# Kernel tuning notes

Measured on AMD Instinct MI355X. Metric: run time of the kernel, lower is better.

The kernel has to match this reference:

```python
import jax, jax.numpy as jnp
import numpy as np

B, T, F, H, OUT, L = 4096, 336, 12, 50, 1, 3


def _lstm_layer(x_tbf, W_ih, W_hh, b_ih, b_hh):
    """PyTorch-semantics LSTM layer. x_tbf: [T,B,in]; returns [T,B,H]."""
    Hh = W_hh.shape[1]
    Bsz = x_tbf.shape[1]
    # precompute input projection for all timesteps: [T,B,4H]
    xz = jnp.einsum('tbf,gf->tbg', x_tbf, W_ih) + (b_ih + b_hh)

    def step(carry, xz_t):
        h, c = carry
        z = xz_t + h @ W_hh.T  # [B,4H]
        i, f, g, o = jnp.split(z, 4, axis=-1)  # PyTorch gate order i,f,g,o
        c = jax.nn.sigmoid(f) * c + jax.nn.sigmoid(i) * jnp.tanh(g)
        h = jax.nn.sigmoid(o) * jnp.tanh(c)
        return (h, c), h

    h0 = jnp.zeros((Bsz, Hh), x_tbf.dtype)
    c0 = jnp.zeros((Bsz, Hh), x_tbf.dtype)
    _, hs = jax.lax.scan(step, (h0, c0), xz)
    return hs


def setup_inputs() -> dict:
    key = jax.random.key(0)
    ks = jax.random.split(key, 16)
    s = 1.0 / np.sqrt(H)  # PyTorch LSTM init scale
    inp = {"x": jax.random.normal(ks[0], (B, T, F), dtype=jnp.float32)}
    in_sizes = [F, H, H]
    k = 1
    for l in range(L):
        inp[f"W_ih_{l}"] = jax.random.uniform(ks[k], (4 * H, in_sizes[l]), jnp.float32, -s, s); k += 1
        inp[f"W_hh_{l}"] = jax.random.uniform(ks[k], (4 * H, H), jnp.float32, -s, s); k += 1
        inp[f"b_ih_{l}"] = jax.random.uniform(ks[k], (4 * H,), jnp.float32, -s, s); k += 1
        inp[f"b_hh_{l}"] = jax.random.uniform(ks[k], (4 * H,), jnp.float32, -s, s); k += 1
    inp["W_lin"] = jax.random.uniform(ks[13], (OUT, H), jnp.float32, -s, s)
    inp["b_lin"] = jax.random.uniform(ks[14], (OUT,), jnp.float32, -s, s)
    return inp


def reference(x, W_ih_0, W_hh_0, b_ih_0, b_hh_0,
              W_ih_1, W_hh_1, b_ih_1, b_hh_1,
              W_ih_2, W_hh_2, b_ih_2, b_hh_2,
              W_lin, b_lin):
    h = jnp.transpose(x, (1, 0, 2))  # [T,B,F] time-major for scan
    params = [(W_ih_0, W_hh_0, b_ih_0, b_hh_0),
              (W_ih_1, W_hh_1, b_ih_1, b_hh_1),
              (W_ih_2, W_hh_2, b_ih_2, b_hh_2)]
    for W_ih, W_hh, bi, bh in params:
        h = _lstm_layer(h, W_ih, W_hh, bi, bh)  # [T,B,H]
    last = h[-1]  # out[:, -1, :] in batch_first layout
    return last @ W_lin.T + b_lin  # [B,OUT]
```

## Files before the change

### kernel.cpp

```cpp
#include <hip/hip_runtime.h>


#define Bsz 4096
#define Tt  336
#define BT  16
#define NTH 1024

typedef _Float16 half8 __attribute__((ext_vector_type(8)));
typedef float    floatx4 __attribute__((ext_vector_type(4)));

struct __align__(16) SMem {
  _Float16 act0[2][BT * 64];
  _Float16 act1[2][BT * 64];
  _Float16 act2[2][BT * 64];
};

__device__ __forceinline__ int offA(int n, int L) {
  return n * 64 + ((((L >> 3) ^ n) & 7) << 3) + (L & 7);
}

__device__ __forceinline__ float lstm_cell(floatx4 z, float& c) {
  float ei = __builtin_amdgcn_exp2f(z[0]);
  float ef = __builtin_amdgcn_exp2f(z[1]);
  float eg = __builtin_amdgcn_exp2f(z[2]);
  float eo = __builtin_amdgcn_exp2f(z[3]);
  float ig = __builtin_amdgcn_rcpf(1.f + ei);
  float fg = __builtin_amdgcn_rcpf(1.f + ef);
  float rg = __builtin_amdgcn_rcpf(1.f + eg);
  float og = __builtin_amdgcn_rcpf(1.f + eo);
  float gg = 1.f - 2.f * rg;
  c = fg * c + ig * gg;
  float ec = __builtin_amdgcn_exp2f(2.885390082f * c);
  float rc = __builtin_amdgcn_rcpf(1.f + ec);
  return og * (1.f - 2.f * rc);
}

__device__ __forceinline__ half8 wfrag2(const float* __restrict__ Wa, int lena,
                                        const float* __restrict__ Wb, int offb,
                                        int lenb, int R, int k0) {
  half8 r = {};
  int u = R >> 2, g = R & 3;
  float sc = (g == 2) ? 2.885390082f : -1.442695041f;
  if (u < 50) {
    int row = g * 50 + u;
#pragma unroll
    for (int j = 0; j < 8; ++j) {
      int k = k0 + j;
      float v = 0.f;
      if (Wa && k < lena)                         v = Wa[row * lena + k];
      else if (Wb && k >= offb && k < offb + lenb) v = Wb[row * lenb + (k - offb)];
      r[j] = (_Float16)(sc * v);
    }
  }
  return r;
}

#define MFMA(a, b, acc) __builtin_amdgcn_mfma_f32_16x16x32_f16((a), (b), (acc), 0, 0, 0)

#define CELLS(NCC, b0, b1, sw)                                          \
  {                                                                     \
    floatx4 z0 = bia[0], z1 = bia[1], z2 = bia[2];                      \
    z0 = MFMA(af[0][0], b0, z0);                                        \
    z1 = MFMA(af[1][0], b0, z1);                                        \
    if (NCC == 3) z2 = MFMA(af[2][0], b0, z2);                          \
    z0 = MFMA(af[0][1], b1, z0);                                        \
    z1 = MFMA(af[1][1], b1, z1);                                        \
    if (NCC == 3) z2 = MFMA(af[2][1], b1, z2);                          \
    float h0v = lstm_cell(z0, cst[0]);                                  \
    float h1v = lstm_cell(z1, cst[1]);                                  \
    if (uokk[0]) (sw)[wo[0]] = (_Float16)h0v;                           \
    if (uokk[1]) (sw)[wo[1]] = (_Float16)h1v;                           \
    if (NCC == 3) {                                                     \
      float h2v = lstm_cell(z2, cst[2]);                                \
      if (uokk[2]) (sw)[wo[2]] = (_Float16)h2v;                         \
    }                                                                   \
  }

#define CELLSD(NCC, b0, b1, pp, sw)                                     \
  {                                                                     \
    floatx4 z0 = bia[0], z1 = bia[1], z2 = bia[2];                      \
    z0 = MFMA(af[0][2], bpf[pp][0], z0);                                \
    z1 = MFMA(af[1][2], bpf[pp][0], z1);                                \
    if (NCC == 3) z2 = MFMA(af[2][2], bpf[pp][0], z2);                  \
    z0 = MFMA(af[0][3], bpf[pp][1], z0);                                \
    z1 = MFMA(af[1][3], bpf[pp][1], z1);                                \
    if (NCC == 3) z2 = MFMA(af[2][3], bpf[pp][1], z2);                  \
    z0 = MFMA(af[0][0], b0, z0);                                        \
    z1 = MFMA(af[1][0], b0, z1);                                        \
    if (NCC == 3) z2 = MFMA(af[2][0], b0, z2);                          \
    z0 = MFMA(af[0][1], b1, z0);                                        \
    z1 = MFMA(af[1][1], b1, z1);                                        \
    if (NCC == 3) z2 = MFMA(af[2][1], b1, z2);                          \
    float h0v = lstm_cell(z0, cst[0]);                                  \
    float h1v = lstm_cell(z1, cst[1]);                                  \
    if (uokk[0]) (sw)[wo[0]] = (_Float16)h0v;                           \
    if (uokk[1]) (sw)[wo[1]] = (_Float16)h1v;                           \
    if (NCC == 3) {                                                     \
      float h2v = lstm_cell(z2, cst[2]);                                \
      if (uokk[2]) (sw)[wo[2]] = (_Float16)h2v;                         \
    }                                                                   \
  }

__global__ __launch_bounds__(NTH, 4)
void lstm_mfma_kernel(const float* __restrict__ x,
                      const float* __restrict__ Wih0, const float* __restrict__ Whh0,
                      const float* __restrict__ bih0, const float* __restrict__ bhh0,
                      const float* __restrict__ Wih1, const float* __restrict__ Whh1,
                      const float* __restrict__ bih1, const float* __restrict__ bhh1,
                      const float* __restrict__ Wih2, const float* __restrict__ Whh2,
                      const float* __restrict__ bih2, const float* __restrict__ bhh2,
                      const float* __restrict__ Wlin, const float* __restrict__ blin,
                      float* __restrict__ out) {
  __shared__ SMem sm;
  const int tid  = threadIdx.x;
  const int blk  = blockIdx.x;
  const int lane = tid & 63;
  const int w    = tid >> 6;
  const int n    = lane & 15;
  const int q    = lane >> 4;

  {
    int* zp = (int*)&sm;
    for (int i = tid; i < (int)(sizeof(SMem) / 4); i += NTH) zp[i] = 0;
  }

  int Lw, nc, mm3[3] = {0, 0, 0};
  switch (w) {
    case 0:  Lw = 0; nc = 3; mm3[0] = 0;  mm3[1] = 1;  mm3[2] = 2;  break;
    case 1:  Lw = 0; nc = 2; mm3[0] = 3;  mm3[1] = 4;               break;
    case 2:  Lw = 0; nc = 3; mm3[0] = 5;  mm3[1] = 6;  mm3[2] = 7;  break;
    case 3:  Lw = 0; nc = 2; mm3[0] = 8;  mm3[1] = 9;               break;
    case 4:  Lw = 1; nc = 2; mm3[0] = 0;  mm3[1] = 1;               break;
    case 5:  Lw = 1; nc = 3; mm3[0] = 2;  mm3[1] = 3;  mm3[2] = 4;  break;
    case 6:  Lw = 1; nc = 2; mm3[0] = 5;  mm3[1] = 6;               break;
    case 7:  Lw = 1; nc = 3; mm3[0] = 7;  mm3[1] = 8;  mm3[2] = 9;  break;
    case 8:  Lw = 2; nc = 3; mm3[0] = 0;  mm3[1] = 1;  mm3[2] = 2;  break;
    case 9:  Lw = 2; nc = 2; mm3[0] = 3;  mm3[1] = 4;               break;
    case 10: Lw = 2; nc = 2; mm3[0] = 5;  mm3[1] = 6;               break;
    case 11: Lw = 2; nc = 2; mm3[0] = 7;  mm3[1] = 8;               break;
    case 12: Lw = 2; nc = 2; mm3[0] = 9;  mm3[1] = 10;              break;
    case 13: Lw = 0; nc = 3; mm3[0] = 10; mm3[1] = 11; mm3[2] = 12; break;
    case 14: Lw = 1; nc = 3; mm3[0] = 10; mm3[1] = 11; mm3[2] = 12; break;
    default: Lw = 2; nc = 2; mm3[0] = 11; mm3[1] = 12;              break;
  }
  const float* Wih = (Lw == 0) ? Wih0 : ((Lw == 1) ? Wih1 : Wih2);
  const float* Whh = (Lw == 0) ? Whh0 : ((Lw == 1) ? Whh1 : Whh2);
  const float* bih = (Lw == 0) ? bih0 : ((Lw == 1) ? bih1 : bih2);
  const float* bhh = (Lw == 0) ? bhh0 : ((Lw == 1) ? bhh1 : bhh2);

  half8  af[3][4];
  floatx4 bia[3];
  float  cst[3] = {0.f, 0.f, 0.f};
  int    wo[3];
  bool   uokk[3];
#pragma unroll
  for (int i = 0; i < 3; ++i) {
    bia[i] = (floatx4){0, 0, 0, 0};
#pragma unroll
    for (int kc = 0; kc < 4; ++kc) af[i][kc] = (half8){};
    int m = mm3[i];
    int u = 4 * m + q;
    int uc = (u < 50) ? u : 49;
    uokk[i] = (i < nc) && (u < 50);
    wo[i] = (Lw == 0) ? offA(n, 12 + uc) : offA(n, uc);
    if (i < nc) {
      int R = 16 * m + n;
      if (Lw == 0) {
#pragma unroll
        for (int kc = 0; kc < 2; ++kc)
          af[i][kc] = wfrag2(Wih, 12, Whh, 12, 50, R, kc * 32 + q * 8);
      } else {
#pragma unroll
        for (int kc = 0; kc < 2; ++kc) {
          af[i][kc] = wfrag2(Whh, 50, nullptr, 0, 0, R, kc * 32 + q * 8);
          af[i][kc + 2] = (Lw == 1)
              ? wfrag2(nullptr, 0, Wih, 12, 50, R, kc * 32 + q * 8)
              : wfrag2(Wih, 50, nullptr, 0, 0, R, kc * 32 + q * 8);
        }
      }
      if (u < 50) {
#pragma unroll
        for (int g = 0; g < 4; ++g) {
          float sc = (g == 2) ? 2.885390082f : -1.442695041f;
          bia[i][g] = sc * (bih[g * 50 + u] + bhh[g * 50 + u]);
        }
      }
    }
  }

  const int ro[2] = { offA(n, q * 8), offA(n, 32 + q * 8) };

  half8 bpf[2][2] = {};

  const int sr = (tid < 192) ? tid / 12 : 0;
  const int sf = (tid < 192) ? tid - sr * 12 : 0;
  const int sxo = offA(sr, sf);
  const float* xp = x + ((size_t)(blk * BT + sr) * Tt) * 12 + sf;
  float xnext = 0.f;

  __syncthreads();
  if (tid < 192) {
    sm.act0[0][sxo] = (_Float16)xp[0];
    xnext = xp[12];
  }
  __syncthreads();

#define TICK(p, TAU, CHK)                                                  \
  {                                                                        \
    if (Lw == 0) {                                                         \
      if (!(CHK) || (TAU) <= 335) {                                        \
        half8 b0 = *(const half8*)&sm.act0[p][ro[0]];                      \
        half8 b1 = *(const half8*)&sm.act0[p][ro[1]];                      \
        _Float16* sw = &sm.act0[1 - (p)][0];                               \
        if (nc == 3) CELLS(3, b0, b1, sw) else CELLS(2, b0, b1, sw)        \
      }                                                                    \
    } else if (Lw == 1) {                                                  \
      half8 b0 = {}, b1 = {};                                              \
      if (!(CHK) || ((TAU) >= 2 && (TAU) <= 337)) {                        \
        b0 = *(const half8*)&sm.act1[p][ro[0]];                            \
        b1 = *(const half8*)&sm.act1[p][ro[1]];                            \
      }                                                                    \
      if (!(CHK) || ((TAU) >= 1 && (TAU) <= 336)) {                        \
        bpf[1 - (p)][0] = *(const half8*)&sm.act0[p][ro[0]];               \
        bpf[1 - (p)][1] = *(const half8*)&sm.act0[p][ro[1]];               \
      }                                                                    \
      if (!(CHK) || ((TAU) >= 2 && (TAU) <= 337)) {                        \
        _Float16* sw = &sm.act1[1 - (p)][0];                               \
        if (nc == 3) CELLSD(3, b0, b1, p, sw) else CELLSD(2, b0, b1, p, sw)\
      }                                                                    \
    } else {                                                               \
      half8 b0 = {}, b1 = {};                                              \
      if (!(CHK) || ((TAU) >= 4 && (TAU) <= 339)) {                        \
        b0 = *(const half8*)&sm.act2[p][ro[0]];                            \
        b1 = *(const half8*)&sm.act2[p][ro[1]];                            \
      }                                                                    \
      if (!(CHK) || ((TAU) >= 3 && (TAU) <= 338)) {                        \
        bpf[1 - (p)][0] = *(const half8*)&sm.act1[p][ro[0]];               \
        bpf[1 - (p)][1] = *(const half8*)&sm.act1[p][ro[1]];               \
      }                                                                    \
      if (!(CHK) || ((TAU) >= 4 && (TAU) <= 339)) {                        \
        _Float16* sw = &sm.act2[1 - (p)][0];                               \
        if (nc == 3) CELLSD(3, b0, b1, p, sw) else CELLSD(2, b0, b1, p, sw)\
      }                                                                    \
    }                                                                      \
    if (tid < 192) {                                                       \
      if ((TAU) + 1 < Tt) sm.act0[1 - (p)][sxo] = (_Float16)xnext;         \
      xnext = ((TAU) + 2 < Tt) ? xp[((TAU) + 2) * 12] : 0.f;               \
    }                                                                      \
    __syncthreads();                                                       \
  }

  TICK(0, 0, 1)
  TICK(1, 1, 1)
  TICK(0, 2, 1)
  TICK(1, 3, 1)
#pragma unroll 1
  for (int t = 4; t < Tt; t += 2) {
    TICK(0, t, 0)
    TICK(1, t + 1, 0)
  }
  TICK(0, 336, 1)
  TICK(1, 337, 1)
  TICK(0, 338, 1)
  TICK(1, 339, 1)
#undef TICK

  if (tid < BT) {
    float s = blin[0];
    for (int uu = 0; uu < 50; ++uu)
      s += Wlin[uu] * (float)sm.act2[0][offA(tid, uu)];
    out[blk * BT + tid] = s;
  }
}

extern "C" void kernel_launch(void* const* d_in, const int* in_sizes, int n_in,
                              void* d_out, int out_size, void* d_ws, size_t ws_size,
                              hipStream_t stream) {
  const float* x    = (const float*)d_in[0];
  const float* Wih0 = (const float*)d_in[1];
  const float* Whh0 = (const float*)d_in[2];
  const float* bih0 = (const float*)d_in[3];
  const float* bhh0 = (const float*)d_in[4];
  const float* Wih1 = (const float*)d_in[5];
  const float* Whh1 = (const float*)d_in[6];
  const float* bih1 = (const float*)d_in[7];
  const float* bhh1 = (const float*)d_in[8];
  const float* Wih2 = (const float*)d_in[9];
  const float* Whh2 = (const float*)d_in[10];
  const float* bih2 = (const float*)d_in[11];
  const float* bhh2 = (const float*)d_in[12];
  const float* Wlin = (const float*)d_in[13];
  const float* blin = (const float*)d_in[14];
  float* outp = (float*)d_out;

  dim3 grid(Bsz / BT);
  dim3 block(NTH);
  lstm_mfma_kernel<<<grid, block, 0, stream>>>(
      x, Wih0, Whh0, bih0, bhh0, Wih1, Whh1, bih1, bhh1,
      Wih2, Whh2, bih2, bhh2, Wlin, blin, outp);
}
```

Measured before the change: 394.3 us.

## Shorten layer wavefront skew and prefetch recurrent operands after barrier

Each layer now reads its recurrent and input-from-below fragments into registers right after the barrier, instead of at the start of the next tick. This lets layers 1 and 2 consume the lower layer's output from the same tick, so the pipeline skew between layers drops from 2 ticks to 1 and the total tick count falls from 340 to 338. The LSTM cell math is also rewritten to merge sigmoid×tanh products into single reciprocals, cutting the number of rcp operations. The risks are extra register pressure from holding the bR buffers and slightly different rounding from the fused reciprocals.

```diff
diff --git a/kernel.cpp b/kernel.cpp
--- a/kernel.cpp
+++ b/kernel.cpp
@@ -24,15 +24,13 @@
   float ef = __builtin_amdgcn_exp2f(z[1]);
   float eg = __builtin_amdgcn_exp2f(z[2]);
   float eo = __builtin_amdgcn_exp2f(z[3]);
-  float ig = __builtin_amdgcn_rcpf(1.f + ei);
-  float fg = __builtin_amdgcn_rcpf(1.f + ef);
-  float rg = __builtin_amdgcn_rcpf(1.f + eg);
-  float og = __builtin_amdgcn_rcpf(1.f + eo);
-  float gg = 1.f - 2.f * rg;
-  c = fg * c + ig * gg;
+  float fg  = __builtin_amdgcn_rcpf(1.f + ef);
+  float itg = (eg - 1.f) *
+              __builtin_amdgcn_rcpf((1.f + ei) * (1.f + eg));
+  c = fg * c + itg;
   float ec = __builtin_amdgcn_exp2f(2.885390082f * c);
-  float rc = __builtin_amdgcn_rcpf(1.f + ec);
-  return og * (1.f - 2.f * rc);
+  return (ec - 1.f) *
+         __builtin_amdgcn_rcpf((1.f + eo) * (1.f + ec));
 }
 
 __device__ __forceinline__ half8 wfrag2(const float* __restrict__ Wa, int lena,
@@ -47,7 +45,7 @@
     for (int j = 0; j < 8; ++j) {
       int k = k0 + j;
       float v = 0.f;
-      if (Wa && k < lena)                         v = Wa[row * lena + k];
+      if (Wa && k < lena)                          v = Wa[row * lena + k];
       else if (Wb && k >= offb && k < offb + lenb) v = Wb[row * lenb + (k - offb)];
       r[j] = (_Float16)(sc * v);
     }
@@ -57,15 +55,15 @@
 
 #define MFMA(a, b, acc) __builtin_amdgcn_mfma_f32_16x16x32_f16((a), (b), (acc), 0, 0, 0)
 
-#define CELLS(NCC, b0, b1, sw)                                          \
+#define CELLS(NCC, pp, sw)                                              \
   {                                                                     \
     floatx4 z0 = bia[0], z1 = bia[1], z2 = bia[2];                      \
-    z0 = MFMA(af[0][0], b0, z0);                                        \
-    z1 = MFMA(af[1][0], b0, z1);                                        \
-    if (NCC == 3) z2 = MFMA(af[2][0], b0, z2);                          \
-    z0 = MFMA(af[0][1], b1, z0);                                        \
-    z1 = MFMA(af[1][1], b1, z1);                                        \
-    if (NCC == 3) z2 = MFMA(af[2][1], b1, z2);                          \
+    z0 = MFMA(af[0][0], bR[pp][0], z0);                                 \
+    z1 = MFMA(af[1][0], bR[pp][0], z1);                                 \
+    if (NCC == 3) z2 = MFMA(af[2][0], bR[pp][0], z2);                   \
+    z0 = MFMA(af[0][1], bR[pp][1], z0);                                 \
+    z1 = MFMA(af[1][1], bR[pp][1], z1);                                 \
+    if (NCC == 3) z2 = MFMA(af[2][1], bR[pp][1], z2);                   \
     float h0v = lstm_cell(z0, cst[0]);                                  \
     float h1v = lstm_cell(z1, cst[1]);                                  \
     if (uokk[0]) (sw)[wo[0]] = (_Float16)h0v;                           \
@@ -76,21 +74,21 @@
     }                                                                   \
   }
 
-#define CELLSD(NCC, b0, b1, pp, sw)                                     \
+#define CELLSD(NCC, pp, sw)                                             \
   {                                                                     \
     floatx4 z0 = bia[0], z1 = bia[1], z2 = bia[2];                      \
-    z0 = MFMA(af[0][2], bpf[pp][0], z0);                                \
-    z1 = MFMA(af[1][2], bpf[pp][0], z1);                                \
-    if (NCC == 3) z2 = MFMA(af[2][2], bpf[pp][0], z2);                  \
-    z0 = MFMA(af[0][3], bpf[pp][1], z0);                                \
-    z1 = MFMA(af[1][3], bpf[pp][1], z1);                                \
-    if (NCC == 3) z2 = MFMA(af[2][3], bpf[pp][1], z2);                  \
-    z0 = MFMA(af[0][0], b0, z0);                                        \
-    z1 = MFMA(af[1][0], b0, z1);                                        \
-    if (NCC == 3) z2 = MFMA(af[2][0], b0, z2);                          \
-    z0 = MFMA(af[0][1], b1, z0);                                        \
-    z1 = MFMA(af[1][1], b1, z1);                                        \
-    if (NCC == 3) z2 = MFMA(af[2][1], b1, z2);                          \
+    z0 = MFMA(af[0][0], bR[pp][0], z0);                                 \
+    z1 = MFMA(af[1][0], bR[pp][0], z1);                                 \
+    if (NCC == 3) z2 = MFMA(af[2][0], bR[pp][0], z2);                   \
+    z0 = MFMA(af[0][1], bR[pp][1], z0);                                 \
+    z1 = MFMA(af[1][1], bR[pp][1], z1);                                 \
+    if (NCC == 3) z2 = MFMA(af[2][1], bR[pp][1], z2);                   \
+    z0 = MFMA(af[0][2], bR[pp][2], z0);                                 \
+    z1 = MFMA(af[1][2], bR[pp][2], z1);                                 \
+    if (NCC == 3) z2 = MFMA(af[2][2], bR[pp][2], z2);                   \
+    z0 = MFMA(af[0][3], bR[pp][3], z0);                                 \
+    z1 = MFMA(af[1][3], bR[pp][3], z1);                                 \
+    if (NCC == 3) z2 = MFMA(af[2][3], bR[pp][3], z2);                   \
     float h0v = lstm_cell(z0, cst[0]);                                  \
     float h1v = lstm_cell(z1, cst[1]);                                  \
     if (uokk[0]) (sw)[wo[0]] = (_Float16)h0v;                           \
@@ -190,7 +188,7 @@
 
   const int ro[2] = { offA(n, q * 8), offA(n, 32 + q * 8) };
 
-  half8 bpf[2][2] = {};
+  half8 bR[2][4] = {};
 
   const int sr = (tid < 192) ? tid / 12 : 0;
   const int sf = (tid < 192) ? tid - sr * 12 : 0;
@@ -205,42 +203,37 @@
   }
   __syncthreads();
 
+  if (Lw == 0) {
+    bR[0][0] = *(const half8*)&sm.act0[0][ro[0]];
+    bR[0][1] = *(const half8*)&sm.act0[0][ro[1]];
+  } else if (Lw == 1) {
+    bR[0][0] = *(const half8*)&sm.act1[0][ro[0]];
+    bR[0][1] = *(const half8*)&sm.act1[0][ro[1]];
+    bR[0][2] = *(const half8*)&sm.act0[0][ro[0]];
+    bR[0][3] = *(const half8*)&sm.act0[0][ro[1]];
+  } else {
+    bR[0][0] = *(const half8*)&sm.act2[0][ro[0]];
+    bR[0][1] = *(const half8*)&sm.act2[0][ro[1]];
+    bR[0][2] = *(const half8*)&sm.act1[0][ro[0]];
+    bR[0][3] = *(const half8*)&sm.act1[0][ro[1]];
+  }
+
 #define TICK(p, TAU, CHK)                                                  \
   {                                                                        \
     if (Lw == 0) {                                                         \
       if (!(CHK) || (TAU) <= 335) {                                        \
-        half8 b0 = *(const half8*)&sm.act0[p][ro[0]];                      \
-        half8 b1 = *(const half8*)&sm.act0[p][ro[1]];                      \
         _Float16* sw = &sm.act0[1 - (p)][0];                               \
-        if (nc == 3) CELLS(3, b0, b1, sw) else CELLS(2, b0, b1, sw)        \
+        if (nc == 3) CELLS(3, p, sw) else CELLS(2, p, sw)                  \
       }                                                                    \
     } else if (Lw == 1) {                                                  \
-      half8 b0 = {}, b1 = {};                                              \
+      if (!(CHK) || ((TAU) >= 1 && (TAU) <= 336)) {                        \
+        _Float16* sw = &sm.act1[1 - (p)][0];                               \
+        if (nc == 3) CELLSD(3, p, sw) else CELLSD(2, p, sw)                \
+      }                                                                    \
+    } else {                                                               \
       if (!(CHK) || ((TAU) >= 2 && (TAU) <= 337)) {                        \
-        b0 = *(const half8*)&sm.act1[p][ro[0]];                            \
-        b1 = *(const half8*)&sm.act1[p][ro[1]];                            \
-      }                                                                    \
-      if (!(CHK) || ((TAU) >= 1 && (TAU) <= 336)) {                        \
-        bpf[1 - (p)][0] = *(const half8*)&sm.act0[p][ro[0]];               \
-        bpf[1 - (p)][1] = *(const half8*)&sm.act0[p][ro[1]];               \
-      }                                                                    \
-      if (!(CHK) || ((TAU) >= 2 && (TAU) <= 337)) {                        \
-        _Float16* sw = &sm.act1[1 - (p)][0];                               \
-        if (nc == 3) CELLSD(3, b0, b1, p, sw) else CELLSD(2, b0, b1, p, sw)\
-      }                                                                    \
-    } else {                                                               \
-      half8 b0 = {}, b1 = {};                                              \
-      if (!(CHK) || ((TAU) >= 4 && (TAU) <= 339)) {                        \
-        b0 = *(const half8*)&sm.act2[p][ro[0]];                            \
-        b1 = *(const half8*)&sm.act2[p][ro[1]];                            \
-      }                                                                    \
-      if (!(CHK) || ((TAU) >= 3 && (TAU) <= 338)) {                        \
-        bpf[1 - (p)][0] = *(const half8*)&sm.act1[p][ro[0]];               \
-        bpf[1 - (p)][1] = *(const half8*)&sm.act1[p][ro[1]];               \
-      }                                                                    \
-      if (!(CHK) || ((TAU) >= 4 && (TAU) <= 339)) {                        \
         _Float16* sw = &sm.act2[1 - (p)][0];                               \
-        if (nc == 3) CELLSD(3, b0, b1, p, sw) else CELLSD(2, b0, b1, p, sw)\
+        if (nc == 3) CELLSD(3, p, sw) else CELLSD(2, p, sw)                \
       }                                                                    \
     }                                                                      \
     if (tid < 192) {                                                       \
@@ -248,21 +241,37 @@
       xnext = ((TAU) + 2 < Tt) ? xp[((TAU) + 2) * 12] : 0.f;               \
     }                                                                      \
     __syncthreads();                                                       \
+    if (Lw == 0) {                                                         \
+      if (!(CHK) || (TAU) <= 334) {                                        \
+        bR[1 - (p)][0] = *(const half8*)&sm.act0[1 - (p)][ro[0]];          \
+        bR[1 - (p)][1] = *(const half8*)&sm.act0[1 - (p)][ro[1]];          \
+      }                                                                    \
+    } else if (Lw == 1) {                                                  \
+      if (!(CHK) || (TAU) <= 335) {                                        \
+        bR[1 - (p)][0] = *(const half8*)&sm.act1[1 - (p)][ro[0]];          \
+        bR[1 - (p)][1] = *(const half8*)&sm.act1[1 - (p)][ro[1]];          \
+        bR[1 - (p)][2] = *(const half8*)&sm.act0[1 - (p)][ro[0]];          \
+        bR[1 - (p)][3] = *(const half8*)&sm.act0[1 - (p)][ro[1]];          \
+      }                                                                    \
+    } else {                                                               \
+      if (!(CHK) || ((TAU) >= 1 && (TAU) <= 336)) {                        \
+        bR[1 - (p)][0] = *(const half8*)&sm.act2[1 - (p)][ro[0]];          \
+        bR[1 - (p)][1] = *(const half8*)&sm.act2[1 - (p)][ro[1]];          \
+        bR[1 - (p)][2] = *(const half8*)&sm.act1[1 - (p)][ro[0]];          \
+        bR[1 - (p)][3] = *(const half8*)&sm.act1[1 - (p)][ro[1]];          \
+      }                                                                    \
+    }                                                                      \
   }
 
   TICK(0, 0, 1)
   TICK(1, 1, 1)
-  TICK(0, 2, 1)
-  TICK(1, 3, 1)
 #pragma unroll 1
-  for (int t = 4; t < Tt; t += 2) {
+  for (int t = 2; t < Tt; t += 2) {
     TICK(0, t, 0)
     TICK(1, t + 1, 0)
   }
   TICK(0, 336, 1)
   TICK(1, 337, 1)
-  TICK(0, 338, 1)
-  TICK(1, 339, 1)
 #undef TICK
 
   if (tid < BT) {
```

Result: slower. 402.8 us (+2.2%).
